# Performance work log

Hardware: AMD Instinct MI355X
Metric: run time of the kernel (lower is better)

## Reference

```python
import jax, jax.numpy as jnp
import numpy as np

B, ST, SK, D, H, HD, MLP, BLK, NRAND = 2, 2048, 2048, 512, 8, 64, 2048, 64, 3


def _bigbird_block_mask(nq, nk, r, rng):
    """Block-level BigBird mask: 3-block window + global first/last blocks + r random blocks/row."""
    bm = np.zeros((nq, nk), dtype=bool)
    for i in range(nq):
        bm[i, max(i - 1, 0):min(i + 2, nk)] = True  # sliding window of 3 blocks
    bm[0, :] = True; bm[-1, :] = True              # global query blocks
    bm[:, 0] = True; bm[:, -1] = True              # global key blocks
    for i in range(nq):
        avail = np.where(~bm[i])[0]
        if avail.size:
            bm[i, rng.choice(avail, size=min(r, avail.size), replace=False)] = True
    return bm


def _masks():
    rng = np.random.RandomState(0)  # connectivity_seed = 0
    nb_q, nb_k = ST // BLK, SK // BLK
    self_bm = _bigbird_block_mask(nb_q, nb_q, NRAND, rng)
    cross_bm = _bigbird_block_mask(nb_q, nb_k, NRAND, rng)
    ones_blk = np.ones((BLK, BLK), dtype=bool)
    self_mask = np.kron(self_bm, ones_blk) & np.tril(np.ones((ST, ST), dtype=bool))  # causal self-attn
    cross_mask = np.kron(cross_bm, ones_blk)
    return jnp.asarray(self_mask), jnp.asarray(cross_mask)


def setup_inputs() -> dict:
    key = jax.random.key(0)
    ks = jax.random.split(key, 12)
    sd = np.float32(1.0 / np.sqrt(D))
    sh = np.float32(1.0 / np.sqrt(H * HD))
    sm = np.float32(1.0 / np.sqrt(MLP))
    self_mask, cross_mask = _masks()
    return dict(
        targets=jax.random.normal(ks[0], (B, ST, D), jnp.float32),
        encoded=jax.random.normal(ks[1], (B, SK, D), jnp.float32),
        ln1_scale=jnp.ones((D,), jnp.float32), ln1_bias=jnp.zeros((D,), jnp.float32),
        ln2_scale=jnp.ones((D,), jnp.float32), ln2_bias=jnp.zeros((D,), jnp.float32),
        ln3_scale=jnp.ones((D,), jnp.float32), ln3_bias=jnp.zeros((D,), jnp.float32),
        wq1=jax.random.normal(ks[2], (D, H, HD), jnp.float32) * sd,
        wk1=jax.random.normal(ks[3], (D, H, HD), jnp.float32) * sd,
        wv1=jax.random.normal(ks[4], (D, H, HD), jnp.float32) * sd,
        wo1=jax.random.normal(ks[5], (H, HD, D), jnp.float32) * sh,
        wq2=jax.random.normal(ks[6], (D, H, HD), jnp.float32) * sd,
        wk2=jax.random.normal(ks[7], (D, H, HD), jnp.float32) * sd,
        wv2=jax.random.normal(ks[8], (D, H, HD), jnp.float32) * sd,
        wo2=jax.random.normal(ks[9], (H, HD, D), jnp.float32) * sh,
        mlp_w1=jax.random.normal(ks[10], (D, MLP), jnp.float32) * sd,
        mlp_b1=jnp.zeros((MLP,), jnp.float32),
        mlp_w2=jax.random.normal(ks[11], (MLP, D), jnp.float32) * sm,
        mlp_b2=jnp.zeros((D,), jnp.float32),
        self_mask=self_mask, cross_mask=cross_mask,
    )


def _ln(x, s, b, eps=1e-6):
    mu = jnp.mean(x, axis=-1, keepdims=True)
    var = jnp.mean(jnp.square(x - mu), axis=-1, keepdims=True)
    return (x - mu) * jax.lax.rsqrt(var + eps) * s + b


def _attn(xq, xkv, wq, wk, wv, wo, mask):
    q = jnp.einsum('bsd,dhk->bshk', xq, wq) * np.float32(1.0 / np.sqrt(HD))
    k = jnp.einsum('bsd,dhk->bshk', xkv, wk)
    v = jnp.einsum('bsd,dhk->bshk', xkv, wv)
    scores = jnp.einsum('bqhd,bkhd->bhqk', q, k)
    scores = jnp.where(mask[None, None], scores, jnp.float32(-1e9))
    w = jax.nn.softmax(scores, axis=-1)
    o = jnp.einsum('bhqk,bkhd->bqhd', w, v)
    return jnp.einsum('bqhd,hdo->bqo', o, wo)


def reference(targets, encoded, ln1_scale, ln1_bias, ln2_scale, ln2_bias, ln3_scale, ln3_bias,
              wq1, wk1, wv1, wo1, wq2, wk2, wv2, wo2,
              mlp_w1, mlp_b1, mlp_w2, mlp_b2, self_mask, cross_mask):
    # causal BigBird self-attention + residual
    x = _ln(targets, ln1_scale, ln1_bias)
    x = _attn(x, x, wq1, wk1, wv1, wo1, self_mask) + targets
    # BigBird cross-attention over encoder output + residual
    y = _ln(x, ln2_scale, ln2_bias)
    y = _attn(y, encoded, wq2, wk2, wv2, wo2, cross_mask) + x
    # MLP block + residual
    z = _ln(y, ln3_scale, ln3_bias)
    z = jax.nn.gelu(z @ mlp_w1 + mlp_b1) @ mlp_w2 + mlp_b2
    return y + z
```

## Files before the change

### kernel.cpp

```cpp
#include <hip/hip_runtime.h>
#include <hip/hip_bf16.h>

#define DEVINL __device__ __forceinline__

namespace {

constexpr int kB = 2, kST = 2048, kSK = 2048, kD = 512, kH = 8, kHD = 64, kMLP = 2048, kBLK = 64;
constexpr int kNBQ = kST / kBLK;
constexpr int kNBK = kSK / kBLK;
constexpr int kROWS = kB * kST;

typedef float f32x4 __attribute__((ext_vector_type(4)));
typedef int i32x4 __attribute__((ext_vector_type(4)));
typedef short bf16x8 __attribute__((ext_vector_type(8)));

DEVINL float bf2f(unsigned short u) { return __uint_as_float(((unsigned)u) << 16); }

DEVINL unsigned short f2bf(float f) {
  __hip_bfloat16 h = __float2bfloat16(f);
  return *reinterpret_cast<unsigned short*>(&h);
}

DEVINL f32x4 mfma16(bf16x8 a, bf16x8 b, f32x4 c) {
  return __builtin_amdgcn_mfma_f32_16x16x32_bf16(a, b, c, 0, 0, 0);
}

DEVINL int swzb(int r) { return (((r & 7) ^ ((r >> 3) & 7)) << 4); }

__global__ __launch_bounds__(256) void tobf_kernel(const void* __restrict__ src, unsigned short* __restrict__ dst,
                                                   int n, const unsigned* __restrict__ probe) {
  const bool bf = (probe[0] == 0x3F803F80u);
  const int stride = gridDim.x * blockDim.x;
  if (bf) {
    const unsigned short* s = (const unsigned short*)src;
    for (int i = blockIdx.x * blockDim.x + threadIdx.x; i < n; i += stride) dst[i] = s[i];
  } else {
    const float* s = (const float*)src;
    for (int i = blockIdx.x * blockDim.x + threadIdx.x; i < n; i += stride) dst[i] = f2bf(s[i]);
  }
}

struct PSrc { const void* s[8]; };
__global__ __launch_bounds__(256) void param_cvt_kernel(PSrc ps, float* __restrict__ dst,
                                                        const unsigned* __restrict__ probe) {
  const bool bf = (probe[0] == 0x3F803F80u);
  const int i = blockIdx.x * blockDim.x + threadIdx.x;
  if (i >= 5632) return;
  int seg, off;
  if (i < 3072) { seg = i >> 9; off = i & 511; }
  else if (i < 5120) { seg = 6; off = i - 3072; }
  else { seg = 7; off = i - 5120; }
  dst[i] = bf ? bf2f(((const unsigned short*)ps.s[seg])[off]) : ((const float*)ps.s[seg])[off];
}

struct TDesc { const void* src; unsigned short* dst; int K, N, start; float alpha; };
struct TPack { TDesc d[10]; };

__global__ __launch_bounds__(256) void transpose_batch_kernel(TPack p, const unsigned* __restrict__ probe) {
  __shared__ float tile[32][33];
  const bool bf = (probe[0] == 0x3F803F80u);
  const int bid = blockIdx.x;
  int di = 0;
#pragma unroll
  for (int i = 1; i < 10; i++)
    if (bid >= p.d[i].start) di = i;
  const TDesc dd = p.d[di];
  const int local = bid - dd.start;
  const int gx = dd.N / 32;
  const int bx = (local % gx) * 32;
  const int by = (local / gx) * 32;
  const int tx = threadIdx.x & 31, ty = threadIdx.x >> 5;
#pragma unroll
  for (int j = 0; j < 4; j++) {
    const int kr = by + ty + j * 8;
    float v;
    if (bf) v = bf2f(((const unsigned short*)dd.src)[(size_t)kr * dd.N + bx + tx]);
    else v = ((const float*)dd.src)[(size_t)kr * dd.N + bx + tx];
    tile[ty + j * 8][tx] = v;
  }
  __syncthreads();
#pragma unroll
  for (int j = 0; j < 4; j++) {
    const int nr = bx + ty + j * 8;
    dd.dst[(size_t)nr * dd.K + by + tx] = f2bf(dd.alpha * tile[tx][ty + j * 8]);
  }
}

DEVINL int mask_fmt(const void* self_mask) {
  const unsigned* sw = (const unsigned*)self_mask;
  unsigned w = sw[32256];
  unsigned w0 = sw[0];
  if (w == 0x01010101u) return 0;
  if (w0 == 0x3F800000u) return 2;
  if (w0 == 0x00003F80u) return 3;
  return 1;
}

DEVINL bool mask_at(const void* m, int r, int c, int fmt) {
  size_t idx = (size_t)r * kSK + c;
  switch (fmt) {
    case 0: return ((const unsigned char*)m)[idx] != 0;
    case 2: return ((const float*)m)[idx] != 0.f;
    case 3: return ((const unsigned short*)m)[idx] != 0;
    default: return ((const int*)m)[idx] != 0;
  }
}

__global__ void mask_kernel(const void* __restrict__ smask, const void* __restrict__ cmask,
                            unsigned char* __restrict__ sbm, unsigned char* __restrict__ cbm) {
  int fmt = mask_fmt(smask);
  int t = blockIdx.x * blockDim.x + threadIdx.x;
  if (t < kNBQ * kNBK) {
    int i = t / kNBK, j = t % kNBK;
    sbm[t] = mask_at(smask, i * kBLK + kBLK - 1, j * kBLK, fmt) ? 1 : 0;
    cbm[t] = mask_at(cmask, i * kBLK, j * kBLK, fmt) ? 1 : 0;
  }
}

__global__ __launch_bounds__(256) void ln_kernel(const void* __restrict__ x, const float* __restrict__ s,
                                                 const float* __restrict__ b, unsigned short* __restrict__ out,
                                                 int raw, const unsigned* __restrict__ probe) {
  const int row = blockIdx.x, t = threadIdx.x;
  float v0, v1;
  if (raw && probe[0] == 0x3F803F80u) {
    const unsigned short* xr = (const unsigned short*)x + (size_t)row * kD;
    v0 = bf2f(xr[t]); v1 = bf2f(xr[t + 256]);
  } else {
    const float* xr = (const float*)x + (size_t)row * kD;
    v0 = xr[t]; v1 = xr[t + 256];
  }
  float sum = v0 + v1;
#pragma unroll
  for (int o = 32; o; o >>= 1) sum += __shfl_xor(sum, o);
  __shared__ float red[4], red2[4];
  const int wid = t >> 6, lane = t & 63;
  if (lane == 0) red[wid] = sum;
  __syncthreads();
  const float mu = (red[0] + red[1] + red[2] + red[3]) * (1.f / 512.f);
  float d0 = v0 - mu, d1 = v1 - mu;
  float vs = d0 * d0 + d1 * d1;
#pragma unroll
  for (int o = 32; o; o >>= 1) vs += __shfl_xor(vs, o);
  if (lane == 0) red2[wid] = vs;
  __syncthreads();
  const float rstd = rsqrtf((red2[0] + red2[1] + red2[2] + red2[3]) * (1.f / 512.f) + 1e-6f);
  out[(size_t)row * kD + t] = f2bf(d0 * rstd * s[t] + b[t]);
  out[(size_t)row * kD + t + 256] = f2bf(d1 * rstd * s[t + 256] + b[t + 256]);
}

DEVINL float gelu_f(float x) {
  float u = 0.7978845608028654f * (x + 0.044715f * x * x * x);
  return 0.5f * x * (1.f + tanhf(u));
}

enum { GEPI_QKV = 0, GEPI_BF16 = 1, GEPI_RESID_RAW = 2, GEPI_RESID = 3, GEPI_GELU = 4, GEPI_FINAL = 5 };

template <int BM, int WM, int WN, int MT, int NT, int EPI>
__global__ __launch_bounds__(256) void mfma_gemm_kernel(
    const unsigned short* __restrict__ A, const unsigned short* __restrict__ Bt,
    void* __restrict__ Cout, int M, int N, int K,
    const float* __restrict__ bias, const void* __restrict__ resid,
    const unsigned* __restrict__ probe) {
  __shared__ __align__(16) unsigned short As[2][BM * 64];
  __shared__ __align__(16) unsigned short Bs[2][128 * 64];
  const int t = threadIdx.x, w = t >> 6, lane = t & 63;
  const int lg = lane >> 4, lc = lane & 15;
  const int wm = w / WN, wn = w % WN;
  const int bm = blockIdx.y * BM, bn = blockIdx.x * 128;

  f32x4 acc[MT][NT];
#pragma unroll
  for (int mt = 0; mt < MT; mt++)
#pragma unroll
    for (int nt = 0; nt < NT; nt++) acc[mt][nt] = f32x4{0.f, 0.f, 0.f, 0.f};

  constexpr int AU = BM / 32;
  const int row0 = t >> 3, part16 = (t & 7) * 16;

  i32x4 ar[AU], br[4];
  auto LOADR = [&](int k0) {
#pragma unroll
    for (int i = 0; i < AU; i++) ar[i] = *(const i32x4*)(A + (size_t)(bm + row0 + i * 32) * K + k0 + (part16 >> 1));
#pragma unroll
    for (int i = 0; i < 4; i++) br[i] = *(const i32x4*)(Bt + (size_t)(bn + row0 + i * 32) * K + k0 + (part16 >> 1));
  };
  auto WRITES = [&](int buf) {
#pragma unroll
    for (int i = 0; i < AU; i++) {
      const int r = row0 + i * 32;
      *(i32x4*)((char*)&As[buf][0] + r * 128 + (part16 ^ swzb(r))) = ar[i];
    }
#pragma unroll
    for (int i = 0; i < 4; i++) {
      const int r = row0 + i * 32;
      *(i32x4*)((char*)&Bs[buf][0] + r * 128 + (part16 ^ swzb(r))) = br[i];
    }
  };
  auto COMPUTE = [&](int buf) {
#pragma unroll
    for (int c = 0; c < 2; c++) {
      bf16x8 af[MT], bfv[NT];
#pragma unroll
      for (int mt = 0; mt < MT; mt++) {
        const int r = wm * (MT * 16) + mt * 16 + lc;
        af[mt] = *(const bf16x8*)((const char*)&As[buf][0] + r * 128 + ((c * 64 + lg * 16) ^ swzb(r)));
      }
#pragma unroll
      for (int nt = 0; nt < NT; nt++) {
        const int r = wn * (NT * 16) + nt * 16 + lc;
        bfv[nt] = *(const bf16x8*)((const char*)&Bs[buf][0] + r * 128 + ((c * 64 + lg * 16) ^ swzb(r)));
      }
#pragma unroll
      for (int mt = 0; mt < MT; mt++)
#pragma unroll
        for (int nt = 0; nt < NT; nt++) acc[mt][nt] = mfma16(af[mt], bfv[nt], acc[mt][nt]);
    }
  };

  LOADR(0);
  WRITES(0);
  for (int k0 = 0; k0 < K; k0 += 128) {
    __syncthreads();
    LOADR(k0 + 64);
    COMPUTE(0);
    WRITES(1);
    __syncthreads();
    if (k0 + 128 < K) LOADR(k0 + 128);
    COMPUTE(1);
    if (k0 + 128 < K) WRITES(0);
  }

  bool prb = false;
  if constexpr (EPI == GEPI_FINAL || EPI == GEPI_RESID_RAW) prb = (probe[0] == 0x3F803F80u);
#pragma unroll
  for (int mt = 0; mt < MT; mt++) {
#pragma unroll
    for (int i = 0; i < 4; i++) {
      const int row = bm + wm * (MT * 16) + mt * 16 + lg * 4 + i;
#pragma unroll
      for (int nt = 0; nt < NT; nt++) {
        const int col = bn + wn * (NT * 16) + nt * 16 + lc;
        const float vv = acc[mt][nt][i];
        const size_t idx = (size_t)row * N + col;
        if constexpr (EPI == GEPI_QKV) {
          ((unsigned short*)Cout)[(size_t)(col >> 9) * kROWS * 512 + (size_t)row * 512 + (col & 511)] = f2bf(vv);
        } else if constexpr (EPI == GEPI_BF16) {
          ((unsigned short*)Cout)[idx] = f2bf(vv);
        } else if constexpr (EPI == GEPI_RESID_RAW) {
          const float rv = prb ? bf2f(((const unsigned short*)resid)[idx]) : ((const float*)resid)[idx];
          ((float*)Cout)[idx] = vv + rv;
        } else if constexpr (EPI == GEPI_RESID) {
          ((float*)Cout)[idx] = vv + ((const float*)resid)[idx];
        } else if constexpr (EPI == GEPI_GELU) {
          ((unsigned short*)Cout)[idx] = f2bf(gelu_f(vv + bias[col]));
        } else {
          const float r = vv + bias[col] + ((const float*)resid)[idx];
          if (prb) ((unsigned short*)Cout)[idx] = f2bf(r);
          else ((float*)Cout)[idx] = r;
        }
      }
    }
  }
}

template <bool CAUSAL>
__global__ __launch_bounds__(1024) void attn_mfma_kernel(
    const unsigned short* __restrict__ q, const unsigned short* __restrict__ k,
    const unsigned short* __restrict__ v, const unsigned char* __restrict__ bm,
    unsigned short* __restrict__ o) {
  __shared__ __align__(16) char smem[65536];
  const int x = blockIdx.x;
  const int b = x & 1;
  const int xx = x >> 1;
  const int qb = (xx & 1) ? (xx >> 1) : (kNBQ - 1 - (xx >> 1));
  const int h = blockIdx.y;
  const int t = threadIdx.x;
  const int g = t >> 8;
  const int tl = t & 255;
  const int w = (t >> 6) & 3;
  const int lane = t & 63, lg = lane >> 4, lc = lane & 15;

  const unsigned char* bmrow = bm + qb * kNBK;
  const unsigned mask = (unsigned)__ballot(lane < kNBK ? (bmrow[lane] != 0) : false);
  const int cnt = __popc(mask);
  const int rounds = (cnt + 3) >> 2;
  unsigned mrem = mask;
  for (int i = 0; i < g; i++) mrem &= mrem - 1;

  const size_t qbase = (((size_t)b * kST + qb * 64 + w * 16 + lc) * kH + h) * kHD;
  const bf16x8 aq0 = *(const bf16x8*)(q + qbase + 8 * lg);
  const bf16x8 aq1 = *(const bf16x8*)(q + qbase + 32 + 8 * lg);

  f32x4 ob[4];
#pragma unroll
  for (int dt = 0; dt < 4; dt++) ob[dt] = f32x4{0.f, 0.f, 0.f, 0.f};
  float mi = -1e30f, li = 0.f;

  char* ksb = smem + g * 8192;
  char* vtb = smem + 32768 + g * 8192;

  const int krr = tl >> 3, kc16 = (tl & 7) * 16;
  const int vkvp = tl >> 3, vdc = (tl & 7) * 8;
  const int vposb = ((vkvp >> 4) << 6) + (((vkvp >> 1) & 3) << 4) + (((vkvp >> 3) & 1) << 3) + ((vkvp & 1) << 2);

  for (int r = 0; r < rounds; r++) {
    const int j = mrem ? (int)__builtin_ctz(mrem) : -1;
#pragma unroll
    for (int i = 0; i < 4; i++) mrem &= mrem - 1;

    if (j >= 0) {
      const size_t kb = (((size_t)b * kSK + j * 64) * kH + h) * kHD;
      const i32x4 kr0 = *(const i32x4*)(k + kb + (size_t)krr * (kH * kHD) + (kc16 >> 1));
      const i32x4 kr1 = *(const i32x4*)(k + kb + (size_t)(krr + 32) * (kH * kHD) + (kc16 >> 1));
      const i32x4 vr0 = *(const i32x4*)(v + kb + (size_t)(2 * vkvp) * (kH * kHD) + vdc);
      const i32x4 vr1 = *(const i32x4*)(v + kb + (size_t)(2 * vkvp + 1) * (kH * kHD) + vdc);
      *(i32x4*)(ksb + krr * 128 + (kc16 ^ swzb(krr))) = kr0;
      *(i32x4*)(ksb + (krr + 32) * 128 + (kc16 ^ swzb(krr + 32))) = kr1;
      union { i32x4 v4; unsigned short u[8]; } a0, a1;
      a0.v4 = vr0; a1.v4 = vr1;
#pragma unroll
      for (int jj = 0; jj < 8; jj++) {
        const int d = vdc + jj;
        const unsigned val = (unsigned)a0.u[jj] | ((unsigned)a1.u[jj] << 16);
        *(unsigned*)(vtb + d * 128 + (vposb ^ swzb(d))) = val;
      }
    }
    __syncthreads();

    if (j >= 0) {
      f32x4 s[4];
#pragma unroll
      for (int t4 = 0; t4 < 4; t4++) s[t4] = f32x4{0.f, 0.f, 0.f, 0.f};
#pragma unroll
      for (int c = 0; c < 2; c++) {
        const bf16x8 aqc = c ? aq1 : aq0;
#pragma unroll
        for (int t4 = 0; t4 < 4; t4++) {
          const int row = t4 * 16 + lc;
          bf16x8 bk = *(const bf16x8*)(ksb + row * 128 + ((c * 64 + lg * 16) ^ swzb(row)));
          s[t4] = mfma16(bk, aqc, s[t4]);
        }
      }

      if (CAUSAL && j == qb) {
#pragma unroll
        for (int t4 = 0; t4 < 4; t4++)
#pragma unroll
          for (int i = 0; i < 4; i++)
            if (t4 * 16 + lg * 4 + i > w * 16 + lc) s[t4][i] = -1e30f;
      }

      float pm = s[0][0];
#pragma unroll
      for (int t4 = 0; t4 < 4; t4++)
#pragma unroll
        for (int i = 0; i < 4; i++) pm = fmaxf(pm, s[t4][i]);
      pm = fmaxf(pm, __shfl_xor(pm, 16));
      pm = fmaxf(pm, __shfl_xor(pm, 32));
      const float mn = fmaxf(mi, pm);
      const float corr = __expf(mi - mn);
      mi = mn;
      float rs = 0.f;
#pragma unroll
      for (int t4 = 0; t4 < 4; t4++)
#pragma unroll
        for (int i = 0; i < 4; i++) {
          s[t4][i] = __expf(s[t4][i] - mn);
          rs += s[t4][i];
        }
      rs += __shfl_xor(rs, 16);
      rs += __shfl_xor(rs, 32);
      li = li * corr + rs;

      float cb[4];
#pragma unroll
      for (int i = 0; i < 4; i++) cb[i] = __shfl(corr, lg * 4 + i);
#pragma unroll
      for (int dt = 0; dt < 4; dt++)
#pragma unroll
        for (int i = 0; i < 4; i++) ob[dt][i] *= cb[i];

      bf16x8 pa[2];
#pragma unroll
      for (int c = 0; c < 2; c++) {
        union { bf16x8 v8; unsigned short u[8]; } pk;
#pragma unroll
        for (int jj = 0; jj < 8; jj++) pk.u[jj] = f2bf(s[2 * c + (jj >> 2)][jj & 3]);
        pa[c] = pk.v8;
      }
#pragma unroll
      for (int c = 0; c < 2; c++)
#pragma unroll
        for (int dt = 0; dt < 4; dt++) {
          const int row = dt * 16 + lc;
          bf16x8 bv = *(const bf16x8*)(vtb + row * 128 + ((c * 64 + lg * 16) ^ swzb(row)));
          ob[dt] = mfma16(pa[c], bv, ob[dt]);
        }
    }
    __syncthreads();
  }

  if (g > 0) {
    float* oc = (float*)smem + (size_t)((g - 1) * 4 + w) * 16 * 64;
#pragma unroll
    for (int dt = 0; dt < 4; dt++)
#pragma unroll
      for (int i = 0; i < 4; i++)
        oc[(lg * 4 + i) * 64 + dt * 16 + lc] = ob[dt][i];
    if (lg == 0) {
      ((float*)(smem + 49152))[((g - 1) * 4 + w) * 16 + lc] = mi;
      ((float*)(smem + 49920))[((g - 1) * 4 + w) * 16 + lc] = li;
    }
  }
  __syncthreads();
  if (g == 0) {
    float mrow[4], lrow[4];
#pragma unroll
    for (int i = 0; i < 4; i++) {
      mrow[i] = __shfl(mi, lg * 4 + i);
      lrow[i] = __shfl(li, lg * 4 + i);
    }
    const float* comb = (const float*)smem;
    const float* cmp = (const float*)(smem + 49152);
    const float* clp = (const float*)(smem + 49920);
    const size_t obase = (((size_t)b * kST + qb * 64 + w * 16) * kH + h) * kHD;
#pragma unroll
    for (int i = 0; i < 4; i++) {
      const int row = lg * 4 + i;
      float M = mrow[i];
      float mg[3];
#pragma unroll
      for (int gi = 0; gi < 3; gi++) {
        mg[gi] = cmp[(gi * 4 + w) * 16 + row];
        M = fmaxf(M, mg[gi]);
      }
      const float wo = __expf(mrow[i] - M);
      float L = lrow[i] * wo;
      float wg[3];
#pragma unroll
      for (int gi = 0; gi < 3; gi++) {
        wg[gi] = __expf(mg[gi] - M);
        L += clp[(gi * 4 + w) * 16 + row] * wg[gi];
      }
      const float inv = 1.0f / L;
#pragma unroll
      for (int dt = 0; dt < 4; dt++) {
        float val = ob[dt][i] * wo;
#pragma unroll
        for (int gi = 0; gi < 3; gi++)
          val += comb[(size_t)((gi * 4 + w) * 16 + row) * 64 + dt * 16 + lc] * wg[gi];
        o[obase + (size_t)row * (kH * kHD) + dt * 16 + lc] = f2bf(val * inv);
      }
    }
  }
}

}

extern "C" void kernel_launch(void* const* d_in, const int* in_sizes, int n_in,
                              void* d_out, int out_size, void* d_ws, size_t ws_size,
                              hipStream_t stream) {
  (void)in_sizes; (void)n_in; (void)out_size; (void)ws_size;
  const unsigned* probe = (const unsigned*)d_in[2];

  char* W = (char*)d_ws;
  size_t off = 0;
  auto allocb = [&](size_t bytes) { char* p = W + off; off += (bytes + 255) & ~size_t(255); return p; };

  float* xbuf = (float*)allocb((size_t)kROWS * kD * 4);
  float* ybuf = (float*)allocb((size_t)kROWS * kD * 4);
  float* f_par = (float*)allocb(5632 * 4);
  float* f_ln[6];
  for (int i = 0; i < 6; i++) f_ln[i] = f_par + i * 512;
  float* f_b1 = f_par + 3072;
  float* f_b2 = f_par + 5120;
  unsigned short* encb = (unsigned short*)allocb((size_t)kROWS * kD * 2);
  unsigned short* lnb  = (unsigned short*)allocb((size_t)kROWS * kD * 2);
  unsigned short* qkvb = (unsigned short*)allocb((size_t)3 * kROWS * kD * 2);
  unsigned short* q2b  = (unsigned short*)allocb((size_t)kROWS * kD * 2);
  unsigned short* kv2b = (unsigned short*)allocb((size_t)2 * kROWS * kD * 2);
  unsigned short* aob  = (unsigned short*)allocb((size_t)kROWS * kD * 2);
  unsigned short* hb16 = (unsigned short*)allocb((size_t)kROWS * kMLP * 2);
  unsigned short* wqkv1 = (unsigned short*)allocb((size_t)3 * 512 * 512 * 2);
  unsigned short* wo1t  = (unsigned short*)allocb((size_t)512 * 512 * 2);
  unsigned short* wq2t  = (unsigned short*)allocb((size_t)512 * 512 * 2);
  unsigned short* wkv2  = (unsigned short*)allocb((size_t)2 * 512 * 512 * 2);
  unsigned short* wo2t  = (unsigned short*)allocb((size_t)512 * 512 * 2);
  unsigned short* w1t   = (unsigned short*)allocb((size_t)2048 * 512 * 2);
  unsigned short* w2t   = (unsigned short*)allocb((size_t)512 * 2048 * 2);
  unsigned char* sbm = (unsigned char*)allocb(kNBQ * kNBK);
  unsigned char* cbm = (unsigned char*)allocb(kNBQ * kNBK);

  tobf_kernel<<<2048, 256, 0, stream>>>(d_in[1], encb, kROWS * kD, probe);
  {
    PSrc ps;
    for (int i = 0; i < 6; i++) ps.s[i] = d_in[2 + i];
    ps.s[6] = d_in[17];
    ps.s[7] = d_in[19];
    param_cvt_kernel<<<22, 256, 0, stream>>>(ps, f_par, probe);
  }
  {
    TPack p;
    const void* srcs[10] = {d_in[8], d_in[9], d_in[10], d_in[11], d_in[12],
                            d_in[13], d_in[14], d_in[15], d_in[16], d_in[18]};
    unsigned short* dsts[10] = {wqkv1, wqkv1 + 512 * 512, wqkv1 + 2 * 512 * 512, wo1t, wq2t,
                                wkv2, wkv2 + 512 * 512, wo2t, w1t, w2t};
    const int Ksz[10] = {512, 512, 512, 512, 512, 512, 512, 512, 512, 2048};
    const int Nsz[10] = {512, 512, 512, 512, 512, 512, 512, 512, 2048, 512};
    int start = 0;
    for (int i = 0; i < 10; i++) {
      p.d[i].src = srcs[i]; p.d[i].dst = dsts[i]; p.d[i].K = Ksz[i]; p.d[i].N = Nsz[i];
      p.d[i].start = start;
      p.d[i].alpha = (i == 0 || i == 4) ? 0.125f : 1.0f;
      start += (Nsz[i] / 32) * (Ksz[i] / 32);
    }
    transpose_batch_kernel<<<start, 256, 0, stream>>>(p, probe);
  }
  mask_kernel<<<1, 1024, 0, stream>>>(d_in[20], d_in[21], sbm, cbm);

  const dim3 blk(256);
  const dim3 blk1k(1024);
  const dim3 g_qkv1(12, 32);
  const dim3 g_kv2(8, 32);
  const dim3 g_mlp1(16, 32);
  const dim3 g_n512(4, 64);
  const dim3 g_attn(kNBQ * kB, kH);

  unsigned short* qb16 = qkvb;
  unsigned short* kb16 = qkvb + (size_t)kROWS * 512;
  unsigned short* vb16 = qkvb + (size_t)2 * kROWS * 512;
  unsigned short* k2b = kv2b;
  unsigned short* v2b = kv2b + (size_t)kROWS * 512;

  ln_kernel<<<kROWS, blk, 0, stream>>>(d_in[0], f_ln[0], f_ln[1], lnb, 1, probe);
  mfma_gemm_kernel<128, 2, 2, 4, 4, GEPI_QKV><<<g_qkv1, blk, 0, stream>>>(lnb, wqkv1, qkvb, kROWS, 1536, 512, nullptr, nullptr, probe);
  attn_mfma_kernel<true><<<g_attn, blk1k, 0, stream>>>(qb16, kb16, vb16, sbm, aob);
  mfma_gemm_kernel<64, 1, 4, 4, 2, GEPI_RESID_RAW><<<g_n512, blk, 0, stream>>>(aob, wo1t, xbuf, kROWS, 512, 512, nullptr, d_in[0], probe);

  ln_kernel<<<kROWS, blk, 0, stream>>>(xbuf, f_ln[2], f_ln[3], lnb, 0, probe);
  mfma_gemm_kernel<64, 1, 4, 4, 2, GEPI_BF16><<<g_n512, blk, 0, stream>>>(lnb, wq2t, q2b, kROWS, 512, 512, nullptr, nullptr, probe);
  mfma_gemm_kernel<128, 2, 2, 4, 4, GEPI_QKV><<<g_kv2, blk, 0, stream>>>(encb, wkv2, kv2b, kROWS, 1024, 512, nullptr, nullptr, probe);
  attn_mfma_kernel<false><<<g_attn, blk1k, 0, stream>>>(q2b, k2b, v2b, cbm, aob);
  mfma_gemm_kernel<64, 1, 4, 4, 2, GEPI_RESID><<<g_n512, blk, 0, stream>>>(aob, wo2t, ybuf, kROWS, 512, 512, nullptr, xbuf, probe);

  ln_kernel<<<kROWS, blk, 0, stream>>>(ybuf, f_ln[4], f_ln[5], lnb, 0, probe);
  mfma_gemm_kernel<128, 2, 2, 4, 4, GEPI_GELU><<<g_mlp1, blk, 0, stream>>>(lnb, w1t, hb16, kROWS, kMLP, 512, f_b1, nullptr, probe);
  mfma_gemm_kernel<64, 1, 4, 4, 2, GEPI_FINAL><<<g_n512, blk, 0, stream>>>(hb16, w2t, d_out, kROWS, 512, 2048, f_b2, ybuf, probe);
}
```

Before: 239.5 us.

## Use direct global-to-LDS loads in GEMM and prefetch K/V in attention

The GEMM staging now uses global_load_lds to copy A/B tiles straight into shared memory, so the register round-trip and XOR swizzle are gone, and LDS reads become unswizzled. The attention kernel loads K fragments directly into registers and skips LDS for K. It software-pipelines the next block's K and V loads behind the current compute, double-buffers the V tile and removes one barrier per round. The risks are more LDS bank conflicts from the unswizzled GEMM layout, higher register pressure from prefetched K fragments under the added launch-bounds hint, and the correctness of the double buffering with only one barrier per round.

```diff
diff --git a/kernel.cpp b/kernel.cpp
--- a/kernel.cpp
+++ b/kernel.cpp
@@ -23,6 +23,11 @@
 
 DEVINL f32x4 mfma16(bf16x8 a, bf16x8 b, f32x4 c) {
   return __builtin_amdgcn_mfma_f32_16x16x32_bf16(a, b, c, 0, 0, 0);
+}
+
+DEVINL void gload16(const void* g, void* l) {
+  __builtin_amdgcn_global_load_lds((const __attribute__((address_space(1))) void*)g,
+                                   (__attribute__((address_space(3))) void*)l, 16, 0, 0);
 }
 
 DEVINL int swzb(int r) { return (((r & 7) ^ ((r >> 3) & 7)) << 4); }
@@ -175,26 +180,17 @@
     for (int nt = 0; nt < NT; nt++) acc[mt][nt] = f32x4{0.f, 0.f, 0.f, 0.f};
 
   constexpr int AU = BM / 32;
-  const int row0 = t >> 3, part16 = (t & 7) * 16;
-
-  i32x4 ar[AU], br[4];
-  auto LOADR = [&](int k0) {
-#pragma unroll
-    for (int i = 0; i < AU; i++) ar[i] = *(const i32x4*)(A + (size_t)(bm + row0 + i * 32) * K + k0 + (part16 >> 1));
-#pragma unroll
-    for (int i = 0; i < 4; i++) br[i] = *(const i32x4*)(Bt + (size_t)(bn + row0 + i * 32) * K + k0 + (part16 >> 1));
-  };
-  auto WRITES = [&](int buf) {
-#pragma unroll
-    for (int i = 0; i < AU; i++) {
-      const int r = row0 + i * 32;
-      *(i32x4*)((char*)&As[buf][0] + r * 128 + (part16 ^ swzb(r))) = ar[i];
-    }
-#pragma unroll
-    for (int i = 0; i < 4; i++) {
-      const int r = row0 + i * 32;
-      *(i32x4*)((char*)&Bs[buf][0] + r * 128 + (part16 ^ swzb(r))) = br[i];
-    }
+  const int row0 = t >> 3, colh = (t & 7) * 8;
+
+  auto STAGE = [&](int buf, int k0) {
+#pragma unroll
+    for (int i = 0; i < AU; i++)
+      gload16(A + (size_t)(bm + row0 + i * 32) * K + k0 + colh,
+              (char*)&As[buf][0] + i * 4096 + t * 16);
+#pragma unroll
+    for (int i = 0; i < 4; i++)
+      gload16(Bt + (size_t)(bn + row0 + i * 32) * K + k0 + colh,
+              (char*)&Bs[buf][0] + i * 4096 + t * 16);
   };
   auto COMPUTE = [&](int buf) {
 #pragma unroll
@@ -203,12 +199,12 @@
 #pragma unroll
       for (int mt = 0; mt < MT; mt++) {
         const int r = wm * (MT * 16) + mt * 16 + lc;
-        af[mt] = *(const bf16x8*)((const char*)&As[buf][0] + r * 128 + ((c * 64 + lg * 16) ^ swzb(r)));
+        af[mt] = *(const bf16x8*)((const char*)&As[buf][0] + r * 128 + c * 64 + lg * 16);
       }
 #pragma unroll
       for (int nt = 0; nt < NT; nt++) {
         const int r = wn * (NT * 16) + nt * 16 + lc;
-        bfv[nt] = *(const bf16x8*)((const char*)&Bs[buf][0] + r * 128 + ((c * 64 + lg * 16) ^ swzb(r)));
+        bfv[nt] = *(const bf16x8*)((const char*)&Bs[buf][0] + r * 128 + c * 64 + lg * 16);
       }
 #pragma unroll
       for (int mt = 0; mt < MT; mt++)
@@ -217,17 +213,14 @@
     }
   };
 
-  LOADR(0);
-  WRITES(0);
+  STAGE(0, 0);
   for (int k0 = 0; k0 < K; k0 += 128) {
     __syncthreads();
-    LOADR(k0 + 64);
+    STAGE(1, k0 + 64);
     COMPUTE(0);
-    WRITES(1);
     __syncthreads();
-    if (k0 + 128 < K) LOADR(k0 + 128);
+    if (k0 + 128 < K) STAGE(0, k0 + 128);
     COMPUTE(1);
-    if (k0 + 128 < K) WRITES(0);
   }
 
   bool prb = false;
@@ -264,7 +257,7 @@
 }
 
 template <bool CAUSAL>
-__global__ __launch_bounds__(1024) void attn_mfma_kernel(
+__global__ __launch_bounds__(1024, 4) void attn_mfma_kernel(
     const unsigned short* __restrict__ q, const unsigned short* __restrict__ k,
     const unsigned short* __restrict__ v, const unsigned char* __restrict__ bm,
     unsigned short* __restrict__ o) {
@@ -286,6 +279,9 @@
   const int rounds = (cnt + 3) >> 2;
   unsigned mrem = mask;
   for (int i = 0; i < g; i++) mrem &= mrem - 1;
+  int jcur = mrem ? (int)__builtin_ctz(mrem) : -1;
+#pragma unroll
+  for (int i = 0; i < 4; i++) mrem &= mrem - 1;
 
   const size_t qbase = (((size_t)b * kST + qb * 64 + w * 16 + lc) * kH + h) * kHD;
   const bf16x8 aq0 = *(const bf16x8*)(q + qbase + 8 * lg);
@@ -296,53 +292,60 @@
   for (int dt = 0; dt < 4; dt++) ob[dt] = f32x4{0.f, 0.f, 0.f, 0.f};
   float mi = -1e30f, li = 0.f;
 
-  char* ksb = smem + g * 8192;
-  char* vtb = smem + 32768 + g * 8192;
-
-  const int krr = tl >> 3, kc16 = (tl & 7) * 16;
   const int vkvp = tl >> 3, vdc = (tl & 7) * 8;
   const int vposb = ((vkvp >> 4) << 6) + (((vkvp >> 1) & 3) << 4) + (((vkvp >> 3) & 1) << 3) + ((vkvp & 1) << 2);
 
+  i32x4 kf0[4], kf1[4];
+  i32x4 vr0, vr1;
+  auto LOADK = [&](int j) {
+    const unsigned short* kp = k + (((size_t)b * kSK + j * 64 + lc) * kH + h) * kHD + lg * 8;
+#pragma unroll
+    for (int t4 = 0; t4 < 4; t4++) {
+      kf0[t4] = *(const i32x4*)(kp + (size_t)(t4 * 16) * (kH * kHD));
+      kf1[t4] = *(const i32x4*)(kp + (size_t)(t4 * 16) * (kH * kHD) + 32);
+    }
+  };
+  auto LOADV = [&](int j) {
+    const size_t kb = (((size_t)b * kSK + j * 64) * kH + h) * kHD;
+    vr0 = *(const i32x4*)(v + kb + (size_t)(2 * vkvp) * (kH * kHD) + vdc);
+    vr1 = *(const i32x4*)(v + kb + (size_t)(2 * vkvp + 1) * (kH * kHD) + vdc);
+  };
+  auto WRITEV = [&](char* vtb) {
+    union { i32x4 v4; unsigned short u[8]; } a0, a1;
+    a0.v4 = vr0; a1.v4 = vr1;
+#pragma unroll
+    for (int jj = 0; jj < 8; jj++) {
+      const int d = vdc + jj;
+      const unsigned val = (unsigned)a0.u[jj] | ((unsigned)a1.u[jj] << 16);
+      *(unsigned*)(vtb + d * 128 + (vposb ^ swzb(d))) = val;
+    }
+  };
+
+  if (jcur >= 0) { LOADK(jcur); LOADV(jcur); }
+  int cur = 0;
   for (int r = 0; r < rounds; r++) {
-    const int j = mrem ? (int)__builtin_ctz(mrem) : -1;
+    const int jnext = mrem ? (int)__builtin_ctz(mrem) : -1;
 #pragma unroll
     for (int i = 0; i < 4; i++) mrem &= mrem - 1;
-
-    if (j >= 0) {
-      const size_t kb = (((size_t)b * kSK + j * 64) * kH + h) * kHD;
-      const i32x4 kr0 = *(const i32x4*)(k + kb + (size_t)krr * (kH * kHD) + (kc16 >> 1));
-      const i32x4 kr1 = *(const i32x4*)(k + kb + (size_t)(krr + 32) * (kH * kHD) + (kc16 >> 1));
-      const i32x4 vr0 = *(const i32x4*)(v + kb + (size_t)(2 * vkvp) * (kH * kHD) + vdc);
-      const i32x4 vr1 = *(const i32x4*)(v + kb + (size_t)(2 * vkvp + 1) * (kH * kHD) + vdc);
-      *(i32x4*)(ksb + krr * 128 + (kc16 ^ swzb(krr))) = kr0;
-      *(i32x4*)(ksb + (krr + 32) * 128 + (kc16 ^ swzb(krr + 32))) = kr1;
-      union { i32x4 v4; unsigned short u[8]; } a0, a1;
-      a0.v4 = vr0; a1.v4 = vr1;
-#pragma unroll
-      for (int jj = 0; jj < 8; jj++) {
-        const int d = vdc + jj;
-        const unsigned val = (unsigned)a0.u[jj] | ((unsigned)a1.u[jj] << 16);
-        *(unsigned*)(vtb + d * 128 + (vposb ^ swzb(d))) = val;
-      }
-    }
+    char* vtb = smem + (g * 2 + cur) * 8192;
+
+    if (jcur >= 0) WRITEV(vtb);
     __syncthreads();
-
-    if (j >= 0) {
+    if (jnext >= 0) LOADV(jnext);
+
+    if (jcur >= 0) {
       f32x4 s[4];
 #pragma unroll
       for (int t4 = 0; t4 < 4; t4++) s[t4] = f32x4{0.f, 0.f, 0.f, 0.f};
 #pragma unroll
-      for (int c = 0; c < 2; c++) {
-        const bf16x8 aqc = c ? aq1 : aq0;
-#pragma unroll
-        for (int t4 = 0; t4 < 4; t4++) {
-          const int row = t4 * 16 + lc;
-          bf16x8 bk = *(const bf16x8*)(ksb + row * 128 + ((c * 64 + lg * 16) ^ swzb(row)));
-          s[t4] = mfma16(bk, aqc, s[t4]);
-        }
-      }
-
-      if (CAUSAL && j == qb) {
+      for (int t4 = 0; t4 < 4; t4++) {
+        s[t4] = mfma16(*(const bf16x8*)&kf0[t4], aq0, s[t4]);
+        s[t4] = mfma16(*(const bf16x8*)&kf1[t4], aq1, s[t4]);
+      }
+      const bool diag = CAUSAL && jcur == qb;
+      if (jnext >= 0) LOADK(jnext);
+
+      if (diag) {
 #pragma unroll
         for (int t4 = 0; t4 < 4; t4++)
 #pragma unroll
@@ -397,8 +400,10 @@
           ob[dt] = mfma16(pa[c], bv, ob[dt]);
         }
     }
-    __syncthreads();
-  }
+    jcur = jnext;
+    cur ^= 1;
+  }
+  __syncthreads();
 
   if (g > 0) {
     float* oc = (float*)smem + (size_t)((g - 1) * 4 + w) * 16 * 64;
```

Measured after the change: 313.8 us. +31.0%, slower.
